# Kernel optimization log

Hardware: AMD Instinct MI355X
Metric: run time of the kernel (lower is better)

## Reference

```python
import jax, jax.numpy as jnp
import numpy as np

HEADS = 8
DIM_HEAD = 64
SCALE = DIM_HEAD ** -0.5


def setup_inputs() -> dict:
    key = jax.random.key(0)
    ks = jax.random.split(key, 5)
    B, N, M, D = 8, 1024, 1024, 512
    inner = HEADS * DIM_HEAD  # 512
    return {
        "x": jax.random.normal(ks[0], (B, N, D), dtype=jnp.float32),
        "context": jax.random.normal(ks[1], (B, M, D), dtype=jnp.float32),
        "Wq": jax.random.normal(ks[2], (D, inner), dtype=jnp.float32) * (D ** -0.5),
        "Wkv": jax.random.normal(ks[3], (D, 2 * inner), dtype=jnp.float32) * (D ** -0.5),
        "Wo": jax.random.normal(ks[4], (inner, D), dtype=jnp.float32) * (inner ** -0.5),
        "bo": jnp.zeros((D,), dtype=jnp.float32),
    }


def reference(x, context, Wq, Wkv, Wo, bo):
    B, N, D = x.shape
    M = context.shape[1]
    q = x @ Wq                      # [B, N, inner]
    kv = context @ Wkv              # [B, M, 2*inner]
    k, v = jnp.split(kv, 2, axis=-1)
    # b n (h d) -> b h n d
    split_heads = lambda t: t.reshape(t.shape[0], t.shape[1], HEADS, DIM_HEAD).transpose(0, 2, 1, 3)
    q, k, v = split_heads(q), split_heads(k), split_heads(v)
    dots = jnp.einsum('bhid,bhjd->bhij', q, k) * SCALE  # [B, H, N, M]
    attn = jax.nn.softmax(dots, axis=-1)
    out = jnp.einsum('bhij,bhjd->bhid', attn, v)        # [B, H, N, d]
    out = out.transpose(0, 2, 1, 3).reshape(B, N, HEADS * DIM_HEAD)
    return out @ Wo + bo            # [B, N, D]
```

## Files before the change

### kernel.cpp

```cpp
#include <hip/hip_runtime.h>
#include <stdint.h>

#define LOG2E 1.44269504088896340736f
#define QSCALE (0.125f * LOG2E)

typedef __bf16 bf16x8 __attribute__((ext_vector_type(8)));
typedef float floatx4 __attribute__((ext_vector_type(4)));

__device__ __forceinline__ unsigned short bfbits(float f) {
  __bf16 h = (__bf16)f;
  return __builtin_bit_cast(unsigned short, h);
}

__device__ __forceinline__ float fast_exp2(float x) {
#if __has_builtin(__builtin_amdgcn_exp2f)
  return __builtin_amdgcn_exp2f(x);
#else
  return exp2f(x);
#endif
}

__device__ __forceinline__ void gl2lds16(const void* g, void* l) {
  __builtin_amdgcn_global_load_lds((const __attribute__((address_space(1))) void*)g,
                                   (__attribute__((address_space(3))) void*)l, 16, 0, 0);
}

__global__ __launch_bounds__(256)
void prep_kernel(const float* __restrict__ Wq, const float* __restrict__ Wkv,
                 const float* __restrict__ Wo,
                 unsigned short* __restrict__ WqT, unsigned short* __restrict__ WkvT,
                 unsigned short* __restrict__ WoT) {
  __shared__ float tile[32][33];
  int t = blockIdx.x;
  int tid = threadIdx.x;
  const float* in; unsigned short* out; int N; int tb;
  if (t < 256)      { in = Wq;  out = WqT;  N = 512;  tb = t; }
  else if (t < 768) { in = Wkv; out = WkvT; N = 1024; tb = t - 256; }
  else              { in = Wo;  out = WoT;  N = 512;  tb = t - 768; }
  const int K = 512;
  int nbx = N / 32;
  int n0 = (tb % nbx) * 32, k0 = (tb / nbx) * 32;
  int tx = tid & 31, ty = tid >> 5;
#pragma unroll
  for (int r = ty; r < 32; r += 8)
    tile[r][tx] = in[(long)(k0 + r) * N + n0 + tx];
  __syncthreads();
#pragma unroll
  for (int r = ty; r < 32; r += 8)
    out[(long)(n0 + r) * K + k0 + tx] = bfbits(tile[tx][r]);
}

__global__ __launch_bounds__(256)
void proj_gemm(const float* __restrict__ Xf, const float* __restrict__ Cf,
               const unsigned short* __restrict__ WqT, const unsigned short* __restrict__ WkvT,
               unsigned short* __restrict__ Qb, unsigned short* __restrict__ Kb,
               unsigned short* __restrict__ Vt) {
  __shared__ unsigned short As[2][128 * 32];
  __shared__ unsigned short Bs[2][128 * 32];

  int idx0 = blockIdx.x;
  int idx = (idx0 & 7) * 96 + (idx0 >> 3);
  const float* A; const unsigned short* Bt;
  long bm, bn; int role;
  if (idx < 256) { role = 0; A = Xf; Bt = WqT;  bn = (long)(idx & 3) * 128; bm = (long)(idx >> 2) * 128; }
  else { int j = idx - 256; role = 1; A = Cf; Bt = WkvT; bn = (long)(j & 7) * 128; bm = (long)(j >> 3) * 128; }

  const int tid = threadIdx.x;
  const int wave = tid >> 6;
  const int lane = tid & 63;
  const int l15 = lane & 15;
  const int q4 = lane >> 4;
  const int wm = (wave & 1) * 64;
  const int wn = (wave >> 1) * 64;
  const int K = 512;

  const int ars = tid >> 1, ahalf = tid & 1;
  const long aF = (bm + ars) * 512 + ahalf * 16;
  int awr[2];
#pragma unroll
  for (int w = 0; w < 2; ++w)
    awr[w] = ars * 32 + (((ahalf * 2 + w) ^ ((ars >> 1) & 3)) * 8);

  int boff[2], lds16b[2];
#pragma unroll
  for (int cc = 0; cc < 2; ++cc) {
    int c = cc * 256 + tid;
    int r = c >> 2, kc = c & 3;
    int gc = kc ^ ((r >> 1) & 3);
    boff[cc] = (int)(bn + r) * K + gc * 8;
    lds16b[cc] = c * 16;
  }
  const int csw = (q4 ^ ((l15 >> 1) & 3)) * 8;
  int arow[4], brow[4];
#pragma unroll
  for (int i = 0; i < 4; ++i) {
    arow[i] = (wm + i * 16 + l15) * 32 + csw;
    brow[i] = (wn + i * 16 + l15) * 32 + csw;
  }

  floatx4 acc[4][4];
#pragma unroll
  for (int i = 0; i < 4; ++i)
#pragma unroll
    for (int j = 0; j < 4; ++j) { acc[i][j][0]=0.f; acc[i][j][1]=0.f; acc[i][j][2]=0.f; acc[i][j][3]=0.f; }

  float4 va[4];

#define PROJ_LOADA(KOFF)                                                   \
  {                                                                        \
    _Pragma("unroll")                                                      \
    for (int w = 0; w < 4; ++w)                                            \
      va[w] = *(const float4*)(A + aF + (KOFF) + w * 4);                   \
  }

#define PROJ_WRITEA(BUF)                                                   \
  {                                                                        \
    _Pragma("unroll")                                                      \
    for (int w = 0; w < 2; ++w) {                                          \
      uint4 pk;                                                            \
      pk.x = (unsigned)bfbits(va[2*w].x) | ((unsigned)bfbits(va[2*w].y) << 16);     \
      pk.y = (unsigned)bfbits(va[2*w].z) | ((unsigned)bfbits(va[2*w].w) << 16);     \
      pk.z = (unsigned)bfbits(va[2*w+1].x) | ((unsigned)bfbits(va[2*w+1].y) << 16); \
      pk.w = (unsigned)bfbits(va[2*w+1].z) | ((unsigned)bfbits(va[2*w+1].w) << 16); \
      *(uint4*)(As[(BUF)] + awr[w]) = pk;                                  \
    }                                                                      \
  }

#define PROJ_STAGEB(BUF, KOFF)                                             \
  {                                                                        \
    _Pragma("unroll")                                                      \
    for (int cc = 0; cc < 2; ++cc)                                         \
      gl2lds16(Bt + boff[cc] + (KOFF), (char*)Bs[(BUF)] + lds16b[cc]);     \
  }

#define PROJ_STEP(T, CUR, DO_STAGE)                                        \
  {                                                                        \
    if (DO_STAGE) { PROJ_LOADA(((T) + 1) * 32); PROJ_STAGEB((CUR) ^ 1, ((T) + 1) * 32); } \
    bf16x8 af[4], bfr[4];                                                  \
    _Pragma("unroll")                                                      \
    for (int i = 0; i < 4; ++i) af[i] = *(const bf16x8*)(As[(CUR)] + arow[i]); \
    _Pragma("unroll")                                                      \
    for (int j = 0; j < 4; ++j) bfr[j] = *(const bf16x8*)(Bs[(CUR)] + brow[j]); \
    _Pragma("unroll")                                                      \
    for (int i = 0; i < 4; ++i)                                            \
      _Pragma("unroll")                                                    \
      for (int j = 0; j < 4; ++j)                                          \
        acc[i][j] = __builtin_amdgcn_mfma_f32_16x16x32_bf16(af[i], bfr[j], acc[i][j], 0, 0, 0); \
    if (DO_STAGE) PROJ_WRITEA((CUR) ^ 1);                                  \
    if ((T) < 15) __syncthreads();                                         \
  }

  PROJ_LOADA(0);
  PROJ_STAGEB(0, 0);
  PROJ_WRITEA(0);
  __syncthreads();
  for (int tt = 0; tt < 8; ++tt) {
    PROJ_STEP(2 * tt, 0, true);
    PROJ_STEP(2 * tt + 1, 1, (tt < 7));
  }
#undef PROJ_STEP
#undef PROJ_STAGEB
#undef PROJ_WRITEA
#undef PROJ_LOADA

  const bool vrole = (role == 1) && (bn >= 512);
#pragma unroll
  for (int i = 0; i < 4; ++i) {
#pragma unroll
    for (int j = 0; j < 4; ++j) {
      long col = bn + wn + j * 16 + l15;
      if (vrole) {
        long h = (col - 512) >> 6, d = col & 63;
        long row0 = bm + wm + i * 16 + q4 * 4;
        long b = row0 >> 10, m0 = row0 & 1023;
        unsigned long long pk = (unsigned long long)bfbits(acc[i][j][0])
                              | ((unsigned long long)bfbits(acc[i][j][1]) << 16)
                              | ((unsigned long long)bfbits(acc[i][j][2]) << 32)
                              | ((unsigned long long)bfbits(acc[i][j][3]) << 48);
        *(unsigned long long*)(Vt + ((b * 8 + h) * 64 + d) * 1024 + m0) = pk;
      } else {
        long h = col >> 6, d = col & 63;
#pragma unroll
        for (int r = 0; r < 4; ++r) {
          long row = bm + wm + i * 16 + q4 * 4 + r;
          long b = row >> 10, n = row & 1023;
          float v = acc[i][j][r];
          if (role == 0) Qb[((b * 8 + h) * 1024 + n) * 64 + d] = bfbits(v * QSCALE);
          else           Kb[((b * 8 + h) * 1024 + n) * 64 + d] = bfbits(v);
        }
      }
    }
  }
}

__global__ __launch_bounds__(512)
void attn_kernel(const unsigned short* __restrict__ Qb,
                 const unsigned short* __restrict__ Kb,
                 const unsigned short* __restrict__ Vt,
                 unsigned short* __restrict__ Ob)
{
  __shared__ unsigned short Ksm[2][4096];
  __shared__ unsigned short Vsm[2][4096];
  __shared__ unsigned short Psm[128 * 64];

  const int tid = threadIdx.x;
  const int wave = tid >> 6;
  const int lane = tid & 63;
  const int l15 = lane & 15;
  const int q4 = lane >> 4;
  const int bid = blockIdx.x;
  const int lin = (bid & 7) * 64 + (bid >> 3);
  const int bh = lin >> 3;
  const int nb = lin & 7;

  const long qrow0 = (long)bh * 1024 + nb * 128 + wave * 16;

  bf16x8 qf[2];
#pragma unroll
  for (int ks = 0; ks < 2; ++ks)
    qf[ks] = *(const bf16x8*)(Qb + (qrow0 + l15) * 64 + ks * 32 + q4 * 8);

  floatx4 acc[4];
#pragma unroll
  for (int d = 0; d < 4; ++d) { acc[d][0]=0.f; acc[d][1]=0.f; acc[d][2]=0.f; acc[d][3]=0.f; }
  float suml = 0.0f;

  const unsigned short* Kbase = Kb + (long)bh * 65536;
  const unsigned short* Vbase = Vt + (long)bh * 65536;
  const int jrow = tid >> 3;
  const int cact = (tid & 7) ^ (jrow & 7);
  const int koff = jrow * 64 + cact * 8;
  const int voff = jrow * 1024 + cact * 8;
  const int myl = tid * 16;

  const int s7 = l15 & 7;
  int kfo[2][4];
  int pao[2];
  int pwo[4];
#pragma unroll
  for (int ks = 0; ks < 2; ++ks) {
#pragma unroll
    for (int jn = 0; jn < 4; ++jn)
      kfo[ks][jn] = (jn * 16 + l15) * 64 + (((ks * 4 + q4) ^ s7) * 8);
    pao[ks] = (wave * 16 + l15) * 64 + (((ks * 4 + q4) ^ s7) * 8);
  }
#pragma unroll
  for (int jn = 0; jn < 4; ++jn)
    pwo[jn] = (wave * 16 + l15) * 64 + (((jn * 2 + (q4 >> 1)) ^ s7) * 8) + (q4 & 1) * 4;

  gl2lds16(Kbase + koff, (char*)Ksm[0] + myl);
  gl2lds16(Vbase + voff, (char*)Vsm[0] + myl);

#define ATTN_TILE(TIDX, CUR, STAGE)                                                          \
  {                                                                                          \
    __syncthreads();                                                                         \
    if (STAGE) {                                                                             \
      gl2lds16(Kbase + ((TIDX) + 1) * 4096 + koff, (char*)Ksm[(CUR) ^ 1] + myl);             \
      gl2lds16(Vbase + ((TIDX) + 1) * 64 + voff, (char*)Vsm[(CUR) ^ 1] + myl);               \
    }                                                                                        \
    floatx4 st[4];                                                                           \
    _Pragma("unroll")                                                                        \
    for (int jn = 0; jn < 4; ++jn) {                                                         \
      st[jn][0] = 0.f; st[jn][1] = 0.f; st[jn][2] = 0.f; st[jn][3] = 0.f;                    \
    }                                                                                        \
    _Pragma("unroll")                                                                        \
    for (int ks = 0; ks < 2; ++ks) {                                                         \
      bf16x8 kfr[4];                                                                         \
      _Pragma("unroll")                                                                      \
      for (int jn = 0; jn < 4; ++jn)                                                         \
        kfr[jn] = *(const bf16x8*)(Ksm[(CUR)] + kfo[ks][jn]);                                \
      __builtin_amdgcn_s_setprio(1);                                                         \
      _Pragma("unroll")                                                                      \
      for (int jn = 0; jn < 4; ++jn)                                                         \
        st[jn] = __builtin_amdgcn_mfma_f32_16x16x32_bf16(kfr[jn], qf[ks], st[jn], 0, 0, 0);  \
      __builtin_amdgcn_s_setprio(0);                                                         \
    }                                                                                        \
    bf16x8 vbt[2][4];        \
    _Pragma("unroll")                                                                        \
    for (int ks = 0; ks < 2; ++ks)                                                           \
      _Pragma("unroll")                                                                      \
      for (int dn = 0; dn < 4; ++dn)                                                         \
        vbt[ks][dn] = *(const bf16x8*)(Vsm[(CUR)] + kfo[ks][dn]);                            \
    _Pragma("unroll")                                                                        \
    for (int jn = 0; jn < 4; ++jn) {                                                         \
      float p0 = fast_exp2(st[jn][0]);                                                       \
      float p1 = fast_exp2(st[jn][1]);                                                       \
      float p2 = fast_exp2(st[jn][2]);                                                       \
      float p3 = fast_exp2(st[jn][3]);                                                       \
      suml += (p0 + p1) + (p2 + p3);                                                         \
      unsigned int lo = (unsigned int)bfbits(p0) | ((unsigned int)bfbits(p1) << 16);         \
      unsigned int hi = (unsigned int)bfbits(p2) | ((unsigned int)bfbits(p3) << 16);         \
      unsigned long long pk = (unsigned long long)lo | ((unsigned long long)hi << 32);       \
      *(unsigned long long*)(Psm + pwo[jn]) = pk;                                            \
    }                                                                                        \
    __asm__ volatile("s_waitcnt lgkmcnt(0)" ::: "memory");                                   \
    _Pragma("unroll")                                                                        \
    for (int ks = 0; ks < 2; ++ks) {                                                         \
      bf16x8 pa = *(const bf16x8*)(Psm + pao[ks]);                                           \
      __builtin_amdgcn_s_setprio(1);                                                         \
      _Pragma("unroll")                                                                      \
      for (int dn = 0; dn < 4; ++dn)                                                         \
        acc[dn] = __builtin_amdgcn_mfma_f32_16x16x32_bf16(pa, vbt[ks][dn], acc[dn], 0, 0, 0);\
      __builtin_amdgcn_s_setprio(0);                                                         \
    }                                                                                        \
  }

  for (int tt = 0; tt < 8; ++tt) {
    ATTN_TILE(2 * tt, 0, true);
    ATTN_TILE(2 * tt + 1, 1, (tt < 7));
  }
#undef ATTN_TILE

  float l = suml;
  l += __shfl_xor(l, 16, 64);
  l += __shfl_xor(l, 32, 64);
  float inv = 1.0f / l;
  float invr[4];
#pragma unroll
  for (int r = 0; r < 4; ++r) invr[r] = __shfl(inv, q4 * 4 + r, 64);

  const int b = bh >> 3, h = bh & 7;
#pragma unroll
  for (int dn = 0; dn < 4; ++dn) {
#pragma unroll
    for (int r = 0; r < 4; ++r) {
      long row = (long)b * 1024 + nb * 128 + wave * 16 + q4 * 4 + r;
      long col = h * 64 + dn * 16 + l15;
      Ob[row * 512 + col] = bfbits(acc[dn][r] * invr[r]);
    }
  }
}

__global__ __launch_bounds__(256)
void out_gemm(const unsigned short* __restrict__ A,
              const unsigned short* __restrict__ Bt,
              float* __restrict__ outF, const float* __restrict__ bias) {
  __shared__ unsigned short As[2][64 * 32];
  __shared__ unsigned short Bs[2][64 * 32];

  int bid = blockIdx.x;
  int swz = (bid & 7) * 128 + (bid >> 3);
  const long bm = (long)(swz >> 3) * 64;
  const long bn = (long)(swz & 7) * 64;

  const int tid = threadIdx.x;
  const int wave = tid >> 6;
  const int lane = tid & 63;
  const int l15 = lane & 15;
  const int q4 = lane >> 4;
  const int wm = (wave & 1) * 32;
  const int wn = (wave >> 1) * 32;
  const int K = 512, N = 512;

  const int r = tid >> 2, kc = tid & 3;
  const int gc = kc ^ ((r >> 1) & 3);
  const int aoff = (int)(bm + r) * K + gc * 8;
  const int boff = (int)(bn + r) * K + gc * 8;
  const int myl = tid * 16;

  const int csw = (q4 ^ ((l15 >> 1) & 3)) * 8;
  int arow[2], brow[2];
#pragma unroll
  for (int i = 0; i < 2; ++i) {
    arow[i] = (wm + i * 16 + l15) * 32 + csw;
    brow[i] = (wn + i * 16 + l15) * 32 + csw;
  }

  floatx4 acc[2][2];
#pragma unroll
  for (int i = 0; i < 2; ++i)
#pragma unroll
    for (int j = 0; j < 2; ++j) { acc[i][j][0]=0.f; acc[i][j][1]=0.f; acc[i][j][2]=0.f; acc[i][j][3]=0.f; }

#define OUT_STAGE(BUF, KOFF)                                        \
  {                                                                 \
    gl2lds16(A + aoff + (KOFF), (char*)As[(BUF)] + myl);            \
    gl2lds16(Bt + boff + (KOFF), (char*)Bs[(BUF)] + myl);           \
  }

#define OUT_STEP(T, CUR, DO_STAGE)                                  \
  {                                                                 \
    if (DO_STAGE) OUT_STAGE((CUR) ^ 1, ((T) + 1) * 32);             \
    bf16x8 af[2], bfr[2];                                           \
    _Pragma("unroll")                                               \
    for (int i = 0; i < 2; ++i) af[i] = *(const bf16x8*)(As[(CUR)] + arow[i]); \
    _Pragma("unroll")                                               \
    for (int j = 0; j < 2; ++j) bfr[j] = *(const bf16x8*)(Bs[(CUR)] + brow[j]); \
    _Pragma("unroll")                                               \
    for (int i = 0; i < 2; ++i)                                     \
      _Pragma("unroll")                                             \
      for (int j = 0; j < 2; ++j)                                   \
        acc[i][j] = __builtin_amdgcn_mfma_f32_16x16x32_bf16(af[i], bfr[j], acc[i][j], 0, 0, 0); \
    if ((T) < 15) __syncthreads();                                  \
  }

  OUT_STAGE(0, 0);
  __syncthreads();
  for (int tt = 0; tt < 8; ++tt) {
    OUT_STEP(2 * tt, 0, true);
    OUT_STEP(2 * tt + 1, 1, (tt < 7));
  }
#undef OUT_STEP
#undef OUT_STAGE

#pragma unroll
  for (int i = 0; i < 2; ++i) {
#pragma unroll
    for (int j = 0; j < 2; ++j) {
      long col = bn + wn + j * 16 + l15;
      float bv = bias[col];
#pragma unroll
      for (int rr = 0; rr < 4; ++rr) {
        long row = bm + wm + i * 16 + q4 * 4 + rr;
        outF[row * (long)N + col] = acc[i][j][rr] + bv;
      }
    }
  }
}

extern "C" void kernel_launch(void* const* d_in, const int* in_sizes, int n_in,
                              void* d_out, int out_size, void* d_ws, size_t ws_size,
                              hipStream_t stream) {
  const float* x   = (const float*)d_in[0];
  const float* ctx = (const float*)d_in[1];
  const float* Wq  = (const float*)d_in[2];
  const float* Wkv = (const float*)d_in[3];
  const float* Wo  = (const float*)d_in[4];
  const float* bo  = (const float*)d_in[5];
  float* out = (float*)d_out;

  char* ws = (char*)d_ws;
  unsigned short* WqT  = (unsigned short*)(ws + (16u << 20));
  unsigned short* WkvT = (unsigned short*)(ws + (17u << 20));
  unsigned short* WoT  = (unsigned short*)(ws + (19u << 20));
  unsigned short* Qb   = (unsigned short*)(ws + (20u << 20));
  unsigned short* Kb   = (unsigned short*)(ws + (28u << 20));
  unsigned short* Vt   = (unsigned short*)(ws + (36u << 20));
  unsigned short* Ob   = (unsigned short*)(ws + (44u << 20));

  prep_kernel<<<1024, 256, 0, stream>>>(Wq, Wkv, Wo, WqT, WkvT, WoT);
  proj_gemm<<<768, 256, 0, stream>>>(x, ctx, WqT, WkvT, Qb, Kb, Vt);
  attn_kernel<<<512, 512, 0, stream>>>(Qb, Kb, Vt, Ob);
  out_gemm<<<1024, 256, 0, stream>>>(Ob, WoT, out, bo);
}
```

Measured before the change: 156.4 us.

## Triple-buffer LDS staging in projection and output GEMMs with partial vmcnt waits

Moves the projection and output GEMMs from double to triple LDS buffering, so tile loads are issued two K-steps ahead. The full __syncthreads drain is replaced by explicit s_waitcnt vmcnt(2) plus s_barrier, which lets one stage of global-to-LDS loads stay in flight across the barrier. The aim is to hide global load latency behind MFMA work. The cost is more LDS per block, which may lower occupancy, and hand-tuned waitcnt counts that depend on how the compiler orders the instructions.

```diff
diff --git a/kernel.cpp b/kernel.cpp
--- a/kernel.cpp
+++ b/kernel.cpp
@@ -55,8 +55,8 @@
                const unsigned short* __restrict__ WqT, const unsigned short* __restrict__ WkvT,
                unsigned short* __restrict__ Qb, unsigned short* __restrict__ Kb,
                unsigned short* __restrict__ Vt) {
-  __shared__ unsigned short As[2][128 * 32];
-  __shared__ unsigned short Bs[2][128 * 32];
+  __shared__ unsigned short As[3][128 * 32];
+  __shared__ unsigned short Bs[3][128 * 32];
 
   int idx0 = blockIdx.x;
   int idx = (idx0 & 7) * 96 + (idx0 >> 3);
@@ -133,31 +133,38 @@
       gl2lds16(Bt + boff[cc] + (KOFF), (char*)Bs[(BUF)] + lds16b[cc]);     \
   }
 
-#define PROJ_STEP(T, CUR, DO_STAGE)                                        \
+#define PROJ_STEP(T, CB, PB)                                               \
   {                                                                        \
-    if (DO_STAGE) { PROJ_LOADA(((T) + 1) * 32); PROJ_STAGEB((CUR) ^ 1, ((T) + 1) * 32); } \
+    if ((T) < 14) { PROJ_LOADA(((T) + 2) * 32); PROJ_STAGEB(PB, ((T) + 2) * 32); } \
     bf16x8 af[4], bfr[4];                                                  \
     _Pragma("unroll")                                                      \
-    for (int i = 0; i < 4; ++i) af[i] = *(const bf16x8*)(As[(CUR)] + arow[i]); \
-    _Pragma("unroll")                                                      \
-    for (int j = 0; j < 4; ++j) bfr[j] = *(const bf16x8*)(Bs[(CUR)] + brow[j]); \
+    for (int i = 0; i < 4; ++i) af[i] = *(const bf16x8*)(As[CB] + arow[i]); \
+    _Pragma("unroll")                                                      \
+    for (int j = 0; j < 4; ++j) bfr[j] = *(const bf16x8*)(Bs[CB] + brow[j]); \
     _Pragma("unroll")                                                      \
     for (int i = 0; i < 4; ++i)                                            \
       _Pragma("unroll")                                                    \
       for (int j = 0; j < 4; ++j)                                          \
         acc[i][j] = __builtin_amdgcn_mfma_f32_16x16x32_bf16(af[i], bfr[j], acc[i][j], 0, 0, 0); \
-    if (DO_STAGE) PROJ_WRITEA((CUR) ^ 1);                                  \
-    if ((T) < 15) __syncthreads();                                         \
-  }
-
-  PROJ_LOADA(0);
-  PROJ_STAGEB(0, 0);
-  PROJ_WRITEA(0);
-  __syncthreads();
-  for (int tt = 0; tt < 8; ++tt) {
-    PROJ_STEP(2 * tt, 0, true);
-    PROJ_STEP(2 * tt + 1, 1, (tt < 7));
-  }
+    if ((T) < 14) PROJ_WRITEA(PB);                                         \
+    if ((T) < 15) {                                                        \
+      if ((T) < 14) { __asm__ volatile("s_waitcnt vmcnt(2) lgkmcnt(0)" ::: "memory"); } \
+      else          { __asm__ volatile("s_waitcnt vmcnt(0) lgkmcnt(0)" ::: "memory"); } \
+      __builtin_amdgcn_s_barrier();                                        \
+    }                                                                      \
+  }
+
+  PROJ_LOADA(0);  PROJ_STAGEB(0, 0);  PROJ_WRITEA(0);
+  PROJ_LOADA(32); PROJ_STAGEB(1, 32); PROJ_WRITEA(1);
+  __asm__ volatile("s_waitcnt vmcnt(2) lgkmcnt(0)" ::: "memory");
+  __builtin_amdgcn_s_barrier();
+
+  for (int tq = 0; tq < 5; ++tq) {
+    PROJ_STEP(3 * tq + 0, 0, 2);
+    PROJ_STEP(3 * tq + 1, 1, 0);
+    PROJ_STEP(3 * tq + 2, 2, 1);
+  }
+  PROJ_STEP(15, 0, 2);
 #undef PROJ_STEP
 #undef PROJ_STAGEB
 #undef PROJ_WRITEA
@@ -335,8 +342,8 @@
 void out_gemm(const unsigned short* __restrict__ A,
               const unsigned short* __restrict__ Bt,
               float* __restrict__ outF, const float* __restrict__ bias) {
-  __shared__ unsigned short As[2][64 * 32];
-  __shared__ unsigned short Bs[2][64 * 32];
+  __shared__ unsigned short As[3][64 * 32];
+  __shared__ unsigned short Bs[3][64 * 32];
 
   int bid = blockIdx.x;
   int swz = (bid & 7) * 128 + (bid >> 3);
@@ -378,28 +385,37 @@
     gl2lds16(Bt + boff + (KOFF), (char*)Bs[(BUF)] + myl);           \
   }
 
-#define OUT_STEP(T, CUR, DO_STAGE)                                  \
+#define OUT_STEP(T, CB, PB)                                         \
   {                                                                 \
-    if (DO_STAGE) OUT_STAGE((CUR) ^ 1, ((T) + 1) * 32);             \
+    if ((T) < 14) OUT_STAGE(PB, ((T) + 2) * 32);                    \
     bf16x8 af[2], bfr[2];                                           \
     _Pragma("unroll")                                               \
-    for (int i = 0; i < 2; ++i) af[i] = *(const bf16x8*)(As[(CUR)] + arow[i]); \
+    for (int i = 0; i < 2; ++i) af[i] = *(const bf16x8*)(As[CB] + arow[i]); \
     _Pragma("unroll")                                               \
-    for (int j = 0; j < 2; ++j) bfr[j] = *(const bf16x8*)(Bs[(CUR)] + brow[j]); \
+    for (int j = 0; j < 2; ++j) bfr[j] = *(const bf16x8*)(Bs[CB] + brow[j]); \
     _Pragma("unroll")                                               \
     for (int i = 0; i < 2; ++i)                                     \
       _Pragma("unroll")                                             \
       for (int j = 0; j < 2; ++j)                                   \
         acc[i][j] = __builtin_amdgcn_mfma_f32_16x16x32_bf16(af[i], bfr[j], acc[i][j], 0, 0, 0); \
-    if ((T) < 15) __syncthreads();                                  \
+    if ((T) < 15) {                                                 \
+      if ((T) < 14) { __asm__ volatile("s_waitcnt vmcnt(2) lgkmcnt(0)" ::: "memory"); } \
+      else          { __asm__ volatile("s_waitcnt vmcnt(0) lgkmcnt(0)" ::: "memory"); } \
+      __builtin_amdgcn_s_barrier();                                 \
+    }                                                               \
   }
 
   OUT_STAGE(0, 0);
-  __syncthreads();
-  for (int tt = 0; tt < 8; ++tt) {
-    OUT_STEP(2 * tt, 0, true);
-    OUT_STEP(2 * tt + 1, 1, (tt < 7));
-  }
+  OUT_STAGE(1, 32);
+  __asm__ volatile("s_waitcnt vmcnt(2) lgkmcnt(0)" ::: "memory");
+  __builtin_amdgcn_s_barrier();
+
+  for (int tq = 0; tq < 5; ++tq) {
+    OUT_STEP(3 * tq + 0, 0, 2);
+    OUT_STEP(3 * tq + 1, 1, 0);
+    OUT_STEP(3 * tq + 2, 2, 1);
+  }
+  OUT_STEP(15, 0, 2);
 #undef OUT_STEP
 #undef OUT_STAGE
 
```

Result: slower. 165.6 us (+5.9%).

## Process two key tiles per barrier in attention and reorder out-GEMM staging

Applied to the files above, without the earlier changes.

The attention loop now double-buffers pairs of 64-key K/V tiles. Two tiles are computed between barriers, which halves the number of __syncthreads and issues prefetches in larger groups. This doubles K/V shared memory per block, which may cut how many blocks fit on a CU. In the output GEMM, the async global-to-LDS stage for the next tile is moved after the current tile's LDS fragment reads, to change how loads and MFMAs are scheduled.

```diff
diff --git a/kernel.cpp b/kernel.cpp
--- a/kernel.cpp
+++ b/kernel.cpp
@@ -199,8 +199,8 @@
                  const unsigned short* __restrict__ Vt,
                  unsigned short* __restrict__ Ob)
 {
-  __shared__ unsigned short Ksm[2][4096];
-  __shared__ unsigned short Vsm[2][4096];
+  __shared__ unsigned short Ksm[2][2][4096];
+  __shared__ unsigned short Vsm[2][2][4096];
   __shared__ unsigned short Psm[128 * 64];
 
   const int tid = threadIdx.x;
@@ -248,16 +248,14 @@
   for (int jn = 0; jn < 4; ++jn)
     pwo[jn] = (wave * 16 + l15) * 64 + (((jn * 2 + (q4 >> 1)) ^ s7) * 8) + (q4 & 1) * 4;
 
-  gl2lds16(Kbase + koff, (char*)Ksm[0] + myl);
-  gl2lds16(Vbase + voff, (char*)Vsm[0] + myl);
-
-#define ATTN_TILE(TIDX, CUR, STAGE)                                                          \
+  gl2lds16(Kbase + koff, (char*)Ksm[0][0] + myl);
+  gl2lds16(Vbase + voff, (char*)Vsm[0][0] + myl);
+  gl2lds16(Kbase + 4096 + koff, (char*)Ksm[0][1] + myl);
+  gl2lds16(Vbase + 64 + voff, (char*)Vsm[0][1] + myl);
+  __syncthreads();
+
+#define ATTN_CHAIN(P, W)                                                                     \
   {                                                                                          \
-    __syncthreads();                                                                         \
-    if (STAGE) {                                                                             \
-      gl2lds16(Kbase + ((TIDX) + 1) * 4096 + koff, (char*)Ksm[(CUR) ^ 1] + myl);             \
-      gl2lds16(Vbase + ((TIDX) + 1) * 64 + voff, (char*)Vsm[(CUR) ^ 1] + myl);               \
-    }                                                                                        \
     floatx4 st[4];                                                                           \
     _Pragma("unroll")                                                                        \
     for (int jn = 0; jn < 4; ++jn) {                                                         \
@@ -268,7 +266,7 @@
       bf16x8 kfr[4];                                                                         \
       _Pragma("unroll")                                                                      \
       for (int jn = 0; jn < 4; ++jn)                                                         \
-        kfr[jn] = *(const bf16x8*)(Ksm[(CUR)] + kfo[ks][jn]);                                \
+        kfr[jn] = *(const bf16x8*)(Ksm[(P)][(W)] + kfo[ks][jn]);                             \
       __builtin_amdgcn_s_setprio(1);                                                         \
       _Pragma("unroll")                                                                      \
       for (int jn = 0; jn < 4; ++jn)                                                         \
@@ -280,7 +278,7 @@
     for (int ks = 0; ks < 2; ++ks)                                                           \
       _Pragma("unroll")                                                                      \
       for (int dn = 0; dn < 4; ++dn)                                                         \
-        vbt[ks][dn] = *(const bf16x8*)(Vsm[(CUR)] + kfo[ks][dn]);                            \
+        vbt[ks][dn] = *(const bf16x8*)(Vsm[(P)][(W)] + kfo[ks][dn]);                         \
     _Pragma("unroll")                                                                        \
     for (int jn = 0; jn < 4; ++jn) {                                                         \
       float p0 = fast_exp2(st[jn][0]);                                                       \
@@ -305,11 +303,25 @@
     }                                                                                        \
   }
 
-  for (int tt = 0; tt < 8; ++tt) {
-    ATTN_TILE(2 * tt, 0, true);
-    ATTN_TILE(2 * tt + 1, 1, (tt < 7));
-  }
-#undef ATTN_TILE
+#define ATTN_SUPER(S, P, STG)                                                                \
+  {                                                                                          \
+    if (STG) {                                                                               \
+      gl2lds16(Kbase + (2 * (S) + 2) * 4096 + koff, (char*)Ksm[(P) ^ 1][0] + myl);           \
+      gl2lds16(Vbase + (2 * (S) + 2) * 64 + voff, (char*)Vsm[(P) ^ 1][0] + myl);             \
+      gl2lds16(Kbase + (2 * (S) + 3) * 4096 + koff, (char*)Ksm[(P) ^ 1][1] + myl);           \
+      gl2lds16(Vbase + (2 * (S) + 3) * 64 + voff, (char*)Vsm[(P) ^ 1][1] + myl);             \
+    }                                                                                        \
+    ATTN_CHAIN(P, 0);                                                                        \
+    ATTN_CHAIN(P, 1);                                                                        \
+    if ((S) < 7) __syncthreads();                                                            \
+  }
+
+  for (int ss = 0; ss < 4; ++ss) {
+    ATTN_SUPER(2 * ss, 0, true);
+    ATTN_SUPER(2 * ss + 1, 1, (ss < 3));
+  }
+#undef ATTN_SUPER
+#undef ATTN_CHAIN
 
   float l = suml;
   l += __shfl_xor(l, 16, 64);
@@ -380,12 +392,12 @@
 
 #define OUT_STEP(T, CUR, DO_STAGE)                                  \
   {                                                                 \
-    if (DO_STAGE) OUT_STAGE((CUR) ^ 1, ((T) + 1) * 32);             \
     bf16x8 af[2], bfr[2];                                           \
     _Pragma("unroll")                                               \
     for (int i = 0; i < 2; ++i) af[i] = *(const bf16x8*)(As[(CUR)] + arow[i]); \
     _Pragma("unroll")                                               \
     for (int j = 0; j < 2; ++j) bfr[j] = *(const bf16x8*)(Bs[(CUR)] + brow[j]); \
+    if (DO_STAGE) OUT_STAGE((CUR) ^ 1, ((T) + 1) * 32);             \
     _Pragma("unroll")                                               \
     for (int i = 0; i < 2; ++i)                                     \
       _Pragma("unroll")                                             \
```

New measurement: 158.3 us. Within noise of the previous version (+1.2%).
